# Performance work log

Measured on AMD Instinct MI355X. Metric: run time of the kernel, lower is better.

Reference implementation:

```python
import jax, jax.numpy as jnp
import numpy as np

H = 10          # hidden_dim
OUT = 100       # linear output (charset logits)
STEPS = 30      # decoder steps
START = 1.0     # Alphabet.start_integer
NL = 3          # num_layers
B, L, TD, AD = 8192, 32, 63, 1
IN = TD + AD


def setup_inputs() -> dict:
    key = jax.random.key(0)
    ks = iter(jax.random.split(key, 64))
    s = 0.3
    d = {}
    d["families"] = jnp.zeros((B,), jnp.int32)
    d["languages"] = jnp.zeros((B,), jnp.int32)
    d["tags"] = jax.random.uniform(next(ks), (B, TD), jnp.float32)
    d["lemmata"] = jax.random.uniform(next(ks), (B, L), jnp.float32)
    for pre in ("enc", "dec"):
        for l in range(NL):
            din = IN if l == 0 else H
            d[f"{pre}_W_ih{l}"] = jax.random.normal(next(ks), (4 * H, din), jnp.float32) * s
            d[f"{pre}_W_hh{l}"] = jax.random.normal(next(ks), (4 * H, H), jnp.float32) * s
            d[f"{pre}_b_ih{l}"] = jax.random.normal(next(ks), (4 * H,), jnp.float32) * s
            d[f"{pre}_b_hh{l}"] = jax.random.normal(next(ks), (4 * H,), jnp.float32) * s
    d["lin_W"] = jax.random.normal(next(ks), (OUT, H), jnp.float32) * s
    d["lin_b"] = jnp.zeros((OUT,), jnp.float32)
    return d


def _lstm_cell(layers, h, c, x):
    # torch LSTM gate order: i, f, g, o. Dropout inactive in eval mode.
    nh, nc, inp = [], [], x
    for (W_ih, W_hh, b_ih, b_hh), hl, cl in zip(layers, h, c):
        g = inp @ W_ih.T + hl @ W_hh.T + b_ih + b_hh  # (B, 4H)
        i_, f_, g_, o_ = jnp.split(g, 4, axis=-1)
        cl = jax.nn.sigmoid(f_) * cl + jax.nn.sigmoid(i_) * jnp.tanh(g_)
        hl = jax.nn.sigmoid(o_) * jnp.tanh(cl)
        nh.append(hl); nc.append(cl); inp = hl
    return tuple(nh), tuple(nc), inp


def _forward(tags, lemmata, enc, dec, lin_W, lin_b):
    Bb, Ll = lemmata.shape
    # time-major encoder input: feature order [char, tags...] -> (L, B, 1+TD)
    xs = jnp.concatenate([lemmata.T[:, :, None],
                          jnp.broadcast_to(tags[None], (Ll, Bb, tags.shape[1]))], axis=-1)
    h = tuple(jnp.zeros((Bb, H), lemmata.dtype) for _ in range(NL))
    c = h

    def estep(carry, x):
        hh, cc = carry
        hh, cc, _ = _lstm_cell(enc, hh, cc, x)
        return (hh, cc), None

    (h, c), _ = jax.lax.scan(estep, (h, c), xs)

    tok = jnp.full((Bb,), START, lemmata.dtype)

    def dstep(carry, _):
        hh, cc, t = carry
        x = jnp.concatenate([t[:, None], tags], axis=-1)  # (B, 1+TD)
        hh, cc, y = _lstm_cell(dec, hh, cc, x)
        probs = jax.nn.sigmoid(y @ lin_W.T + lin_b)       # (B, 100)
        nt = jax.lax.stop_gradient(jnp.argmax(probs, axis=-1))
        return (hh, cc, nt.astype(t.dtype)), (probs, nt)

    _, (probs, toks) = jax.lax.scan(dstep, (h, c, tok), None, length=STEPS)
    return jnp.transpose(probs, (1, 0, 2)), toks.T  # (B,30,100), (B,30)


def reference(families, languages, tags, lemmata,
              enc_W_ih0, enc_W_hh0, enc_b_ih0, enc_b_hh0,
              enc_W_ih1, enc_W_hh1, enc_b_ih1, enc_b_hh1,
              enc_W_ih2, enc_W_hh2, enc_b_ih2, enc_b_hh2,
              dec_W_ih0, dec_W_hh0, dec_b_ih0, dec_b_hh0,
              dec_W_ih1, dec_W_hh1, dec_b_ih1, dec_b_hh1,
              dec_W_ih2, dec_W_hh2, dec_b_ih2, dec_b_hh2,
              lin_W, lin_b):
    enc = ((enc_W_ih0, enc_W_hh0, enc_b_ih0, enc_b_hh0),
           (enc_W_ih1, enc_W_hh1, enc_b_ih1, enc_b_hh1),
           (enc_W_ih2, enc_W_hh2, enc_b_ih2, enc_b_hh2))
    dec = ((dec_W_ih0, dec_W_hh0, dec_b_ih0, dec_b_hh0),
           (dec_W_ih1, dec_W_hh1, dec_b_ih1, dec_b_hh1),
           (dec_W_ih2, dec_W_hh2, dec_b_ih2, dec_b_hh2))
    return _forward(tags, lemmata, enc, dec, lin_W, lin_b)
```

## Files before the change

### kernel.cpp

```cpp
#include <hip/hip_runtime.h>
#include <cmath>
#include <stdint.h>

#define DEV __device__ __forceinline__

typedef float v2f __attribute__((ext_vector_type(2)));

static DEV float fast_exp2(float x) { return __builtin_amdgcn_exp2f(x); }
static DEV float fast_rcp(float x) { return __builtin_amdgcn_rcpf(x); }

#define LOG2E 1.4426950408889634f

static DEV float rdl(float x, int l) {
  return __int_as_float(__builtin_amdgcn_readlane(__float_as_int(x), l));
}
static DEV int rdli(float x, int l) {
  return __builtin_amdgcn_readlane(__float_as_int(x), l);
}
static DEV uint64_t pack2(int lo, int hi) {
  return ((uint64_t)(uint32_t)hi << 32) | (uint32_t)lo;
}

static DEV void pkfma(v2f& acc, v2f w, uint64_t h) {
  asm("v_pk_fma_f32 %0, %1, %2, %0" : "+v"(acc) : "v"(w), "s"(h));
}

template <int K>
static DEV float qb(float x) {
  return __int_as_float(
      __builtin_amdgcn_update_dpp(0, __float_as_int(x), K * 0x55, 0xF, 0xF, true));
}

template <int CTRL>
static DEV float dppmax(float x) {
  float o = __int_as_float(
      __builtin_amdgcn_update_dpp(0, __float_as_int(x), CTRL, 0xF, 0xF, true));
  return fmaxf(x, o);
}

static DEV float wavemax_bcast(float m) {
  m = dppmax<0x111>(m);
  m = dppmax<0x112>(m);
  m = dppmax<0x114>(m);
  m = dppmax<0x118>(m);
  m = dppmax<0x142>(m);
  m = dppmax<0x143>(m);
  return rdl(m, 63);
}

struct KP {
  const float* tags; const float* lem;
  const float* eWih0; const float* eWhh0; const float* ebih0; const float* ebhh0;
  const float* eWih1; const float* eWhh1; const float* ebih1; const float* ebhh1;
  const float* eWih2; const float* eWhh2; const float* ebih2; const float* ebhh2;
  const float* dWih0; const float* dWhh0; const float* dbih0; const float* dbhh0;
  const float* dWih1; const float* dWhh1; const float* dbih1; const float* dbhh1;
  const float* dWih2; const float* dWhh2; const float* dbih2; const float* dbhh2;
  const float* linW; const float* linb;
  float* outp; float* outt;
  int B;
};

__global__ __launch_bounds__(256) void seq2seq_kernel(KP P) {
  const int tid = threadIdx.x;
  const int lane = tid & 63;
  const int b = blockIdx.x * 4 + (tid >> 6);
  if (b >= P.B) return;

  const int jq = lane >> 2;
  const int kg = lane & 3;
  const int jj = (jq < 10) ? jq : 9;
  const int row = kg * 10 + jj;

  const float kc = (kg == 2) ? (-2.0f * LOG2E) : (-LOG2E);
  const float am = (kg == 2) ? 2.0f : 1.0f;
  const float ab = (kg == 2) ? -1.0f : 0.0f;

  auto act = [&](float g) -> float {
    float y = fast_rcp(1.0f + fast_exp2(g));
    return fmaf(am, y, ab);
  };

  float tv = (lane < 63) ? P.tags[(size_t)b * 63 + lane] : 0.0f;
  float lemv = (lane < 32) ? P.lem[(size_t)b * 32 + lane] : 0.0f;

  float pre0 = P.ebih0[row] + P.ebhh0[row];
  float dpre0 = P.dbih0[row] + P.dbhh0[row];
  float ew0c, dw0c;
  {
    const float4* e4 = (const float4*)P.eWih0 + row * 16;
    const float4* d4 = (const float4*)P.dWih0 + row * 16;
    float4 we = e4[0], wd = d4[0];
    ew0c = we.x; dw0c = wd.x;
    float t0 = rdl(tv, 0), t1 = rdl(tv, 1), t2 = rdl(tv, 2);
    pre0 = fmaf(we.y, t0, pre0); pre0 = fmaf(we.z, t1, pre0); pre0 = fmaf(we.w, t2, pre0);
    dpre0 = fmaf(wd.y, t0, dpre0); dpre0 = fmaf(wd.z, t1, dpre0); dpre0 = fmaf(wd.w, t2, dpre0);
#pragma unroll
    for (int c = 1; c < 16; c++) {
      float4 e = e4[c], d = d4[c];
      int dd = 4 * c - 1;
      float u0 = rdl(tv, dd), u1 = rdl(tv, dd + 1), u2 = rdl(tv, dd + 2), u3 = rdl(tv, dd + 3);
      pre0 = fmaf(e.x, u0, pre0); pre0 = fmaf(e.y, u1, pre0);
      pre0 = fmaf(e.z, u2, pre0); pre0 = fmaf(e.w, u3, pre0);
      dpre0 = fmaf(d.x, u0, dpre0); dpre0 = fmaf(d.y, u1, dpre0);
      dpre0 = fmaf(d.z, u2, dpre0); dpre0 = fmaf(d.w, u3, dpre0);
    }
    pre0 *= kc; dpre0 *= kc; ew0c *= kc; dw0c *= kc;
  }

  v2f ehh0[5], eih1[5], ehh1[5], eih2[5], ehh2[5];
  {
    const v2f* a0 = (const v2f*)(P.eWhh0 + row * 10);
    const v2f* a1 = (const v2f*)(P.eWih1 + row * 10);
    const v2f* a2 = (const v2f*)(P.eWhh1 + row * 10);
    const v2f* a3 = (const v2f*)(P.eWih2 + row * 10);
    const v2f* a4 = (const v2f*)(P.eWhh2 + row * 10);
#pragma unroll
    for (int q = 0; q < 5; q++) {
      ehh0[q] = a0[q] * kc; eih1[q] = a1[q] * kc; ehh1[q] = a2[q] * kc;
      eih2[q] = a3[q] * kc; ehh2[q] = a4[q] * kc;
    }
  }
  float pre1 = (P.ebih1[row] + P.ebhh1[row]) * kc;
  float pre2 = (P.ebih2[row] + P.ebhh2[row]) * kc;

  uint64_t h0[5], h1[5], h2[5];
#pragma unroll
  for (int q = 0; q < 5; q++) { h0[q] = 0; h1[q] = 0; h2[q] = 0; }
  float c0 = 0.0f, c1 = 0.0f, c2 = 0.0f;

  auto upd = [&](float a, float& c, uint64_t (&h)[5]) {
    float a0 = qb<0>(a);
    float a1 = qb<1>(a);
    float a2 = qb<2>(a);
    float a3 = qb<3>(a);
    c = fmaf(a1, c, a0 * a2);
    float y = fast_rcp(1.0f + fast_exp2(c * (-2.0f * LOG2E)));
    float hv = a3 * fmaf(2.0f, y, -1.0f);
#pragma unroll
    for (int q = 0; q < 5; q++) h[q] = pack2(rdli(hv, 8 * q), rdli(hv, 8 * q + 4));
  };

  auto tdot = [&](const v2f (&w)[5], const uint64_t (&h)[5]) -> float {
    v2f ta{0.0f, 0.0f}, tb{0.0f, 0.0f};
    pkfma(ta, w[0], h[0]); pkfma(tb, w[1], h[1]);
    pkfma(ta, w[2], h[2]); pkfma(tb, w[3], h[3]);
    pkfma(ta, w[4], h[4]);
    return (ta.x + ta.y) + (tb.x + tb.y);
  };

  auto step = [&](float x) {
    v2f s0{pre0, 0.0f}, s1{pre1, 0.0f}, s2{pre2, 0.0f};
#pragma unroll
    for (int q = 0; q < 5; q++) {
      pkfma(s0, ehh0[q], h0[q]);
      pkfma(s1, ehh1[q], h1[q]);
      pkfma(s2, ehh2[q], h2[q]);
    }
    upd(act(fmaf(ew0c, x, s0.x + s0.y)), c0, h0);
    upd(act((s1.x + s1.y) + tdot(eih1, h0)), c1, h1);
    upd(act((s2.x + s2.y) + tdot(eih2, h1)), c2, h2);
  };

#pragma unroll 2
  for (int t = 0; t < 32; t++) step(rdl(lemv, t));

  {
    const v2f* a0 = (const v2f*)(P.dWhh0 + row * 10);
    const v2f* a1 = (const v2f*)(P.dWih1 + row * 10);
    const v2f* a2 = (const v2f*)(P.dWhh1 + row * 10);
    const v2f* a3 = (const v2f*)(P.dWih2 + row * 10);
    const v2f* a4 = (const v2f*)(P.dWhh2 + row * 10);
#pragma unroll
    for (int q = 0; q < 5; q++) {
      ehh0[q] = a0[q] * kc; eih1[q] = a1[q] * kc; ehh1[q] = a2[q] * kc;
      eih2[q] = a3[q] * kc; ehh2[q] = a4[q] * kc;
    }
  }
  pre1 = (P.dbih1[row] + P.dbhh1[row]) * kc;
  pre2 = (P.dbih2[row] + P.dbhh2[row]) * kc;

  const int lr2 = (lane < 36) ? (64 + lane) : 99;
  v2f lw0[5], lw1[5];
  {
    const v2f* a0 = (const v2f*)(P.linW + lane * 10);
    const v2f* a1 = (const v2f*)(P.linW + lr2 * 10);
#pragma unroll
    for (int q = 0; q < 5; q++) { lw0[q] = a0[q] * (-LOG2E); lw1[q] = a1[q] * (-LOG2E); }
  }
  float lb0 = P.linb[lane] * (-LOG2E);
  float lb1 = ((lane < 36) ? P.linb[lr2] : -1e30f) * (-LOG2E);

  float* op0 = P.outp + (size_t)b * 3000;
  float tok = 1.0f;
  float tokv = 0.0f;

  v2f sp0{dpre0, 0.0f}, sp1{pre1, 0.0f}, sp2{pre2, 0.0f};
#pragma unroll
  for (int q = 0; q < 5; q++) {
    pkfma(sp0, ehh0[q], h0[q]);
    pkfma(sp1, ehh1[q], h1[q]);
    pkfma(sp2, ehh2[q], h2[q]);
  }

#pragma unroll 2
  for (int s = 0; s < 30; s++) {
    upd(act(fmaf(dw0c, tok, sp0.x + sp0.y)), c0, h0);
    upd(act((sp1.x + sp1.y) + tdot(eih1, h0)), c1, h1);
    upd(act((sp2.x + sp2.y) + tdot(eih2, h1)), c2, h2);

    sp0 = v2f{dpre0, 0.0f}; sp1 = v2f{pre1, 0.0f}; sp2 = v2f{pre2, 0.0f};
#pragma unroll
    for (int q = 0; q < 5; q++) {
      pkfma(sp0, ehh0[q], h0[q]);
      pkfma(sp1, ehh1[q], h1[q]);
      pkfma(sp2, ehh2[q], h2[q]);
    }

    v2f za{lb0, 0.0f}, zb{lb1, 0.0f};
#pragma unroll
    for (int q = 0; q < 5; q++) { pkfma(za, lw0[q], h2[q]); pkfma(zb, lw1[q], h2[q]); }
    float p0 = fast_rcp(1.0f + fast_exp2(za.x + za.y));
    float p1 = fast_rcp(1.0f + fast_exp2(zb.x + zb.y));

    float* op = op0 + s * 100;
    op[lane] = p0;
    if (lane < 36) op[64 + lane] = p1;

    float vm = wavemax_bcast(fmaxf(p0, p1));
    unsigned long long m0 = __ballot(p0 == vm);
    unsigned long long m1 = __ballot(p1 == vm);
    int im = m0 ? (int)__builtin_ctzll(m0) : 64 + (int)__builtin_ctzll(m1);
    tok = (float)im;
    tokv = (lane == s) ? tok : tokv;
  }

  if (lane < 30) P.outt[(size_t)b * 30 + lane] = tokv;
}

extern "C" void kernel_launch(void* const* d_in, const int* in_sizes, int n_in,
                              void* d_out, int out_size, void* d_ws, size_t ws_size,
                              hipStream_t stream) {
  KP P;
  P.tags = (const float*)d_in[2];
  P.lem = (const float*)d_in[3];
  P.eWih0 = (const float*)d_in[4];  P.eWhh0 = (const float*)d_in[5];
  P.ebih0 = (const float*)d_in[6];  P.ebhh0 = (const float*)d_in[7];
  P.eWih1 = (const float*)d_in[8];  P.eWhh1 = (const float*)d_in[9];
  P.ebih1 = (const float*)d_in[10]; P.ebhh1 = (const float*)d_in[11];
  P.eWih2 = (const float*)d_in[12]; P.eWhh2 = (const float*)d_in[13];
  P.ebih2 = (const float*)d_in[14]; P.ebhh2 = (const float*)d_in[15];
  P.dWih0 = (const float*)d_in[16]; P.dWhh0 = (const float*)d_in[17];
  P.dbih0 = (const float*)d_in[18]; P.dbhh0 = (const float*)d_in[19];
  P.dWih1 = (const float*)d_in[20]; P.dWhh1 = (const float*)d_in[21];
  P.dbih1 = (const float*)d_in[22]; P.dbhh1 = (const float*)d_in[23];
  P.dWih2 = (const float*)d_in[24]; P.dWhh2 = (const float*)d_in[25];
  P.dbih2 = (const float*)d_in[26]; P.dbhh2 = (const float*)d_in[27];
  P.linW = (const float*)d_in[28];
  P.linb = (const float*)d_in[29];

  const int B = in_sizes[3] / 32;
  P.B = B;
  P.outp = (float*)d_out;
  P.outt = P.outp + (size_t)B * 3000;

  const int blocks = (B + 3) / 4;
  seq2seq_kernel<<<dim3(blocks), dim3(256), 0, stream>>>(P);
}
```

Baseline: 151.8 us.

## Interleave two batch elements per wavefront to expose ILP in LSTM recurrence

Each wavefront now runs the encoder and decoder recurrences for two batch elements at once, interleaving their independent LSTM updates, logits and argmax. Weight registers are shared between the two elements and the grid is halved. The aim is to fill the latency of the serial readlane/transcendental dependency chain with independent work. In exchange, register pressure rises, occupancy per SIMD drops, and the loop unroll pragmas are removed.

```diff
diff --git a/kernel.cpp b/kernel.cpp
--- a/kernel.cpp
+++ b/kernel.cpp
@@ -64,8 +64,11 @@
 __global__ __launch_bounds__(256) void seq2seq_kernel(KP P) {
   const int tid = threadIdx.x;
   const int lane = tid & 63;
-  const int b = blockIdx.x * 4 + (tid >> 6);
-  if (b >= P.B) return;
+  int bA = blockIdx.x * 8 + (tid >> 6) * 2;
+  int bB = bA + 1;
+  const bool vA = (bA < P.B), vB = (bB < P.B);
+  if (!vA) bA = P.B - 1;
+  if (!vB) bB = P.B - 1;
 
   const int jq = lane >> 2;
   const int kg = lane & 3;
@@ -81,31 +84,45 @@
     return fmaf(am, y, ab);
   };
 
-  float tv = (lane < 63) ? P.tags[(size_t)b * 63 + lane] : 0.0f;
-  float lemv = (lane < 32) ? P.lem[(size_t)b * 32 + lane] : 0.0f;
-
-  float pre0 = P.ebih0[row] + P.ebhh0[row];
-  float dpre0 = P.dbih0[row] + P.dbhh0[row];
+  float tvA = (lane < 63) ? P.tags[(size_t)bA * 63 + lane] : 0.0f;
+  float tvB = (lane < 63) ? P.tags[(size_t)bB * 63 + lane] : 0.0f;
+  float lemA = (lane < 32) ? P.lem[(size_t)bA * 32 + lane] : 0.0f;
+  float lemB = (lane < 32) ? P.lem[(size_t)bB * 32 + lane] : 0.0f;
+
+  float ebias = P.ebih0[row] + P.ebhh0[row];
+  float dbias = P.dbih0[row] + P.dbhh0[row];
+  float pre0A = ebias, pre0B = ebias, dpre0A = dbias, dpre0B = dbias;
   float ew0c, dw0c;
   {
     const float4* e4 = (const float4*)P.eWih0 + row * 16;
     const float4* d4 = (const float4*)P.dWih0 + row * 16;
     float4 we = e4[0], wd = d4[0];
     ew0c = we.x; dw0c = wd.x;
-    float t0 = rdl(tv, 0), t1 = rdl(tv, 1), t2 = rdl(tv, 2);
-    pre0 = fmaf(we.y, t0, pre0); pre0 = fmaf(we.z, t1, pre0); pre0 = fmaf(we.w, t2, pre0);
-    dpre0 = fmaf(wd.y, t0, dpre0); dpre0 = fmaf(wd.z, t1, dpre0); dpre0 = fmaf(wd.w, t2, dpre0);
+    {
+      float a0 = rdl(tvA, 0), a1 = rdl(tvA, 1), a2 = rdl(tvA, 2);
+      float b0 = rdl(tvB, 0), b1 = rdl(tvB, 1), b2 = rdl(tvB, 2);
+      pre0A = fmaf(we.y, a0, pre0A); pre0A = fmaf(we.z, a1, pre0A); pre0A = fmaf(we.w, a2, pre0A);
+      pre0B = fmaf(we.y, b0, pre0B); pre0B = fmaf(we.z, b1, pre0B); pre0B = fmaf(we.w, b2, pre0B);
+      dpre0A = fmaf(wd.y, a0, dpre0A); dpre0A = fmaf(wd.z, a1, dpre0A); dpre0A = fmaf(wd.w, a2, dpre0A);
+      dpre0B = fmaf(wd.y, b0, dpre0B); dpre0B = fmaf(wd.z, b1, dpre0B); dpre0B = fmaf(wd.w, b2, dpre0B);
+    }
 #pragma unroll
     for (int c = 1; c < 16; c++) {
       float4 e = e4[c], d = d4[c];
       int dd = 4 * c - 1;
-      float u0 = rdl(tv, dd), u1 = rdl(tv, dd + 1), u2 = rdl(tv, dd + 2), u3 = rdl(tv, dd + 3);
-      pre0 = fmaf(e.x, u0, pre0); pre0 = fmaf(e.y, u1, pre0);
-      pre0 = fmaf(e.z, u2, pre0); pre0 = fmaf(e.w, u3, pre0);
-      dpre0 = fmaf(d.x, u0, dpre0); dpre0 = fmaf(d.y, u1, dpre0);
-      dpre0 = fmaf(d.z, u2, dpre0); dpre0 = fmaf(d.w, u3, dpre0);
-    }
-    pre0 *= kc; dpre0 *= kc; ew0c *= kc; dw0c *= kc;
+      float a0 = rdl(tvA, dd), a1 = rdl(tvA, dd + 1), a2 = rdl(tvA, dd + 2), a3 = rdl(tvA, dd + 3);
+      float b0 = rdl(tvB, dd), b1 = rdl(tvB, dd + 1), b2 = rdl(tvB, dd + 2), b3 = rdl(tvB, dd + 3);
+      pre0A = fmaf(e.x, a0, pre0A); pre0A = fmaf(e.y, a1, pre0A);
+      pre0A = fmaf(e.z, a2, pre0A); pre0A = fmaf(e.w, a3, pre0A);
+      pre0B = fmaf(e.x, b0, pre0B); pre0B = fmaf(e.y, b1, pre0B);
+      pre0B = fmaf(e.z, b2, pre0B); pre0B = fmaf(e.w, b3, pre0B);
+      dpre0A = fmaf(d.x, a0, dpre0A); dpre0A = fmaf(d.y, a1, dpre0A);
+      dpre0A = fmaf(d.z, a2, dpre0A); dpre0A = fmaf(d.w, a3, dpre0A);
+      dpre0B = fmaf(d.x, b0, dpre0B); dpre0B = fmaf(d.y, b1, dpre0B);
+      dpre0B = fmaf(d.z, b2, dpre0B); dpre0B = fmaf(d.w, b3, dpre0B);
+    }
+    pre0A *= kc; pre0B *= kc; dpre0A *= kc; dpre0B *= kc;
+    ew0c *= kc; dw0c *= kc;
   }
 
   v2f ehh0[5], eih1[5], ehh1[5], eih2[5], ehh2[5];
@@ -124,10 +141,14 @@
   float pre1 = (P.ebih1[row] + P.ebhh1[row]) * kc;
   float pre2 = (P.ebih2[row] + P.ebhh2[row]) * kc;
 
-  uint64_t h0[5], h1[5], h2[5];
-#pragma unroll
-  for (int q = 0; q < 5; q++) { h0[q] = 0; h1[q] = 0; h2[q] = 0; }
-  float c0 = 0.0f, c1 = 0.0f, c2 = 0.0f;
+  uint64_t h0A[5], h1A[5], h2A[5], h0B[5], h1B[5], h2B[5];
+#pragma unroll
+  for (int q = 0; q < 5; q++) {
+    h0A[q] = 0; h1A[q] = 0; h2A[q] = 0;
+    h0B[q] = 0; h1B[q] = 0; h2B[q] = 0;
+  }
+  float cA0 = 0.0f, cA1 = 0.0f, cA2 = 0.0f;
+  float cB0 = 0.0f, cB1 = 0.0f, cB2 = 0.0f;
 
   auto upd = [&](float a, float& c, uint64_t (&h)[5]) {
     float a0 = qb<0>(a);
@@ -149,21 +170,24 @@
     return (ta.x + ta.y) + (tb.x + tb.y);
   };
 
-  auto step = [&](float x) {
-    v2f s0{pre0, 0.0f}, s1{pre1, 0.0f}, s2{pre2, 0.0f};
-#pragma unroll
-    for (int q = 0; q < 5; q++) {
-      pkfma(s0, ehh0[q], h0[q]);
-      pkfma(s1, ehh1[q], h1[q]);
-      pkfma(s2, ehh2[q], h2[q]);
-    }
-    upd(act(fmaf(ew0c, x, s0.x + s0.y)), c0, h0);
-    upd(act((s1.x + s1.y) + tdot(eih1, h0)), c1, h1);
-    upd(act((s2.x + s2.y) + tdot(eih2, h1)), c2, h2);
+  auto stepAB = [&](float xA, float xB) {
+    v2f s0A{pre0A, 0.0f}, s1A{pre1, 0.0f}, s2A{pre2, 0.0f};
+    v2f s0B{pre0B, 0.0f}, s1B{pre1, 0.0f}, s2B{pre2, 0.0f};
+#pragma unroll
+    for (int q = 0; q < 5; q++) {
+      pkfma(s0A, ehh0[q], h0A[q]); pkfma(s0B, ehh0[q], h0B[q]);
+      pkfma(s1A, ehh1[q], h1A[q]); pkfma(s1B, ehh1[q], h1B[q]);
+      pkfma(s2A, ehh2[q], h2A[q]); pkfma(s2B, ehh2[q], h2B[q]);
+    }
+    upd(act(fmaf(ew0c, xA, s0A.x + s0A.y)), cA0, h0A);
+    upd(act(fmaf(ew0c, xB, s0B.x + s0B.y)), cB0, h0B);
+    upd(act((s1A.x + s1A.y) + tdot(eih1, h0A)), cA1, h1A);
+    upd(act((s1B.x + s1B.y) + tdot(eih1, h0B)), cB1, h1B);
+    upd(act((s2A.x + s2A.y) + tdot(eih2, h1A)), cA2, h2A);
+    upd(act((s2B.x + s2B.y) + tdot(eih2, h1B)), cB2, h2B);
   };
 
-#pragma unroll 2
-  for (int t = 0; t < 32; t++) step(rdl(lemv, t));
+  for (int t = 0; t < 32; t++) stepAB(rdl(lemA, t), rdl(lemB, t));
 
   {
     const v2f* a0 = (const v2f*)(P.dWhh0 + row * 10);
@@ -191,51 +215,75 @@
   float lb0 = P.linb[lane] * (-LOG2E);
   float lb1 = ((lane < 36) ? P.linb[lr2] : -1e30f) * (-LOG2E);
 
-  float* op0 = P.outp + (size_t)b * 3000;
-  float tok = 1.0f;
-  float tokv = 0.0f;
-
-  v2f sp0{dpre0, 0.0f}, sp1{pre1, 0.0f}, sp2{pre2, 0.0f};
+  float* opA = P.outp + (size_t)bA * 3000;
+  float* opB = P.outp + (size_t)bB * 3000;
+  float tokA = 1.0f, tokB = 1.0f;
+  float tokvA = 0.0f, tokvB = 0.0f;
+
+  v2f sp0A{dpre0A, 0.0f}, sp1A{pre1, 0.0f}, sp2A{pre2, 0.0f};
+  v2f sp0B{dpre0B, 0.0f}, sp1B{pre1, 0.0f}, sp2B{pre2, 0.0f};
 #pragma unroll
   for (int q = 0; q < 5; q++) {
-    pkfma(sp0, ehh0[q], h0[q]);
-    pkfma(sp1, ehh1[q], h1[q]);
-    pkfma(sp2, ehh2[q], h2[q]);
-  }
-
-#pragma unroll 2
+    pkfma(sp0A, ehh0[q], h0A[q]); pkfma(sp0B, ehh0[q], h0B[q]);
+    pkfma(sp1A, ehh1[q], h1A[q]); pkfma(sp1B, ehh1[q], h1B[q]);
+    pkfma(sp2A, ehh2[q], h2A[q]); pkfma(sp2B, ehh2[q], h2B[q]);
+  }
+
   for (int s = 0; s < 30; s++) {
-    upd(act(fmaf(dw0c, tok, sp0.x + sp0.y)), c0, h0);
-    upd(act((sp1.x + sp1.y) + tdot(eih1, h0)), c1, h1);
-    upd(act((sp2.x + sp2.y) + tdot(eih2, h1)), c2, h2);
-
-    sp0 = v2f{dpre0, 0.0f}; sp1 = v2f{pre1, 0.0f}; sp2 = v2f{pre2, 0.0f};
-#pragma unroll
-    for (int q = 0; q < 5; q++) {
-      pkfma(sp0, ehh0[q], h0[q]);
-      pkfma(sp1, ehh1[q], h1[q]);
-      pkfma(sp2, ehh2[q], h2[q]);
-    }
-
-    v2f za{lb0, 0.0f}, zb{lb1, 0.0f};
-#pragma unroll
-    for (int q = 0; q < 5; q++) { pkfma(za, lw0[q], h2[q]); pkfma(zb, lw1[q], h2[q]); }
-    float p0 = fast_rcp(1.0f + fast_exp2(za.x + za.y));
-    float p1 = fast_rcp(1.0f + fast_exp2(zb.x + zb.y));
-
-    float* op = op0 + s * 100;
-    op[lane] = p0;
-    if (lane < 36) op[64 + lane] = p1;
-
-    float vm = wavemax_bcast(fmaxf(p0, p1));
-    unsigned long long m0 = __ballot(p0 == vm);
-    unsigned long long m1 = __ballot(p1 == vm);
-    int im = m0 ? (int)__builtin_ctzll(m0) : 64 + (int)__builtin_ctzll(m1);
-    tok = (float)im;
-    tokv = (lane == s) ? tok : tokv;
-  }
-
-  if (lane < 30) P.outt[(size_t)b * 30 + lane] = tokv;
+    upd(act(fmaf(dw0c, tokA, sp0A.x + sp0A.y)), cA0, h0A);
+    upd(act(fmaf(dw0c, tokB, sp0B.x + sp0B.y)), cB0, h0B);
+    upd(act((sp1A.x + sp1A.y) + tdot(eih1, h0A)), cA1, h1A);
+    upd(act((sp1B.x + sp1B.y) + tdot(eih1, h0B)), cB1, h1B);
+    upd(act((sp2A.x + sp2A.y) + tdot(eih2, h1A)), cA2, h2A);
+    upd(act((sp2B.x + sp2B.y) + tdot(eih2, h1B)), cB2, h2B);
+
+    sp0A = v2f{dpre0A, 0.0f}; sp1A = v2f{pre1, 0.0f}; sp2A = v2f{pre2, 0.0f};
+    sp0B = v2f{dpre0B, 0.0f}; sp1B = v2f{pre1, 0.0f}; sp2B = v2f{pre2, 0.0f};
+#pragma unroll
+    for (int q = 0; q < 5; q++) {
+      pkfma(sp0A, ehh0[q], h0A[q]); pkfma(sp0B, ehh0[q], h0B[q]);
+      pkfma(sp1A, ehh1[q], h1A[q]); pkfma(sp1B, ehh1[q], h1B[q]);
+      pkfma(sp2A, ehh2[q], h2A[q]); pkfma(sp2B, ehh2[q], h2B[q]);
+    }
+
+    v2f zaA{lb0, 0.0f}, zbA{lb1, 0.0f}, zaB{lb0, 0.0f}, zbB{lb1, 0.0f};
+#pragma unroll
+    for (int q = 0; q < 5; q++) {
+      pkfma(zaA, lw0[q], h2A[q]); pkfma(zbA, lw1[q], h2A[q]);
+      pkfma(zaB, lw0[q], h2B[q]); pkfma(zbB, lw1[q], h2B[q]);
+    }
+    float p0A = fast_rcp(1.0f + fast_exp2(zaA.x + zaA.y));
+    float p1A = fast_rcp(1.0f + fast_exp2(zbA.x + zbA.y));
+    float p0B = fast_rcp(1.0f + fast_exp2(zaB.x + zaB.y));
+    float p1B = fast_rcp(1.0f + fast_exp2(zbB.x + zbB.y));
+
+    if (vA) {
+      float* op = opA + s * 100;
+      op[lane] = p0A;
+      if (lane < 36) op[64 + lane] = p1A;
+    }
+    if (vB) {
+      float* op = opB + s * 100;
+      op[lane] = p0B;
+      if (lane < 36) op[64 + lane] = p1B;
+    }
+
+    float vmA = wavemax_bcast(fmaxf(p0A, p1A));
+    float vmB = wavemax_bcast(fmaxf(p0B, p1B));
+    unsigned long long m0A = __ballot(p0A == vmA);
+    unsigned long long m1A = __ballot(p1A == vmA);
+    unsigned long long m0B = __ballot(p0B == vmB);
+    unsigned long long m1B = __ballot(p1B == vmB);
+    int imA = m0A ? (int)__builtin_ctzll(m0A) : 64 + (int)__builtin_ctzll(m1A);
+    int imB = m0B ? (int)__builtin_ctzll(m0B) : 64 + (int)__builtin_ctzll(m1B);
+    tokA = (float)imA;
+    tokB = (float)imB;
+    tokvA = (lane == s) ? tokA : tokvA;
+    tokvB = (lane == s) ? tokB : tokvB;
+  }
+
+  if (lane < 30 && vA) P.outt[(size_t)bA * 30 + lane] = tokvA;
+  if (lane < 30 && vB) P.outt[(size_t)bB * 30 + lane] = tokvB;
 }
 
 extern "C" void kernel_launch(void* const* d_in, const int* in_sizes, int n_in,
@@ -264,6 +312,6 @@
   P.outp = (float*)d_out;
   P.outt = P.outp + (size_t)B * 3000;
 
-  const int blocks = (B + 3) / 4;
+  const int blocks = (B + 7) / 8;
   seq2seq_kernel<<<dim3(blocks), dim3(256), 0, stream>>>(P);
 }
```

Result: slower. 160.5 us (+5.7%).
